# Optimization experiments

Measured on AMD Instinct MI355X. Metric: run time of the kernel, lower is better.

Reference implementation:

```python
import jax, jax.numpy as jnp
import numpy as np

D_MODEL = 1024
NUM_HEADS = 16
D_HEAD = D_MODEL // NUM_HEADS


def setup_inputs() -> dict:
    key = jax.random.key(0)
    ks = jax.random.split(key, 9)
    s = 1.0 / np.sqrt(D_MODEL)
    x = jax.random.normal(ks[0], (2, 2048, D_MODEL), dtype=jnp.float32)
    # Linear layers: weight [out, in] (torch convention), bias [out]
    w_q = jax.random.uniform(ks[1], (D_MODEL, D_MODEL), jnp.float32, -s, s)
    b_q = jax.random.uniform(ks[2], (D_MODEL,), jnp.float32, -s, s)
    w_k = jax.random.uniform(ks[3], (D_MODEL, D_MODEL), jnp.float32, -s, s)
    b_k = jax.random.uniform(ks[4], (D_MODEL,), jnp.float32, -s, s)
    w_v = jax.random.uniform(ks[5], (D_MODEL, D_MODEL), jnp.float32, -s, s)
    b_v = jax.random.uniform(ks[6], (D_MODEL,), jnp.float32, -s, s)
    w_o = jax.random.uniform(ks[7], (D_MODEL, D_MODEL), jnp.float32, -s, s)
    b_o = jax.random.uniform(ks[8], (D_MODEL,), jnp.float32, -s, s)
    return {"x": x, "w_q": w_q, "b_q": b_q, "w_k": w_k, "b_k": b_k,
            "w_v": w_v, "b_v": b_v, "w_o": w_o, "b_o": b_o}


def _split_heads(t, b, s):
    # [b, s, d_model] -> [b, h, s, d_head]
    return t.reshape(b, s, NUM_HEADS, D_HEAD).transpose(0, 2, 1, 3)


def reference(x, w_q, b_q, w_k, b_k, w_v, b_v, w_o, b_o):
    b, s, _ = x.shape
    q = _split_heads(x @ w_q.T + b_q, b, s)
    k = _split_heads(x @ w_k.T + b_k, b, s)
    v = _split_heads(x @ w_v.T + b_v, b, s)
    scores = jnp.einsum('bhid,bhjd->bhij', q, k) / jnp.sqrt(jnp.float32(D_HEAD)).astype(x.dtype)
    attn = jax.nn.softmax(scores, axis=-1)
    out = jnp.einsum('bhij,bhjd->bhid', attn, v)
    out = out.transpose(0, 2, 1, 3).reshape(b, s, D_MODEL)
    return out @ w_o.T + b_o
```

## Files before the change

### kernel.cpp

```cpp
#include <hip/hip_runtime.h>
#include <cstddef>
#include <cstdint>
#include <cmath>

#define NH   16
#define DH   64
#define SLEN 2048
#define DM   1024

typedef __bf16          bf16x8   __attribute__((ext_vector_type(8)));
typedef float           f32x4    __attribute__((ext_vector_type(4)));
typedef unsigned short  ushort8  __attribute__((ext_vector_type(8)));
typedef unsigned short  ushort4v __attribute__((ext_vector_type(4)));

__device__ __forceinline__ unsigned short f2bf(float x) {
    union { float f; unsigned u; } v; v.f = x;
    unsigned r = v.u + 0x7fffu + ((v.u >> 16) & 1u);
    return (unsigned short)(r >> 16);
}
__device__ __forceinline__ float bf2f(unsigned short h) {
    union { unsigned u; float f; } v; v.u = ((unsigned)h) << 16;
    return v.f;
}

__device__ __forceinline__ f32x4 mfma16(ushort8 a, ushort8 b, f32x4 c) {
    return __builtin_amdgcn_mfma_f32_16x16x32_bf16(
        __builtin_bit_cast(bf16x8, a), __builtin_bit_cast(bf16x8, b), c, 0, 0, 0);
}

__global__ __launch_bounds__(256)
void convert_hilo(const float* __restrict__ x,
                  const float* __restrict__ wq, const float* __restrict__ wk,
                  const float* __restrict__ wv, const float* __restrict__ wo,
                  unsigned short* __restrict__ xh, unsigned short* __restrict__ xl,
                  unsigned short* __restrict__ wh, unsigned short* __restrict__ wl)
{
    const unsigned c = blockIdx.x * 256 + threadIdx.x;
    const float* src;
    unsigned short *dh, *dl;
    size_t off;
    if (c < 1048576u) {
        src = x; dh = xh; dl = xl; off = c;
    } else {
        unsigned t = c - 1048576u;
        unsigned wsel = t >> 18;
        off = t & 262143u;
        src  = (wsel == 0) ? wq : (wsel == 1) ? wk : (wsel == 2) ? wv : wo;
        dh = wh + ((size_t)wsel << 20);
        dl = wl + ((size_t)wsel << 20);
    }
    float4 v = *(const float4*)(src + off * 4);
    float a[4] = {v.x, v.y, v.z, v.w};
    ushort4v h, l;
    #pragma unroll
    for (int i = 0; i < 4; ++i) {
        unsigned short hi = f2bf(a[i]);
        h[i] = hi;
        l[i] = f2bf(a[i] - bf2f(hi));
    }
    *(ushort4v*)(dh + off * 4) = h;
    *(ushort4v*)(dl + off * 4) = l;
}

template<int MODE>
__global__ __launch_bounds__(256, 1)
void gemm_split(const unsigned short* __restrict__ Ahi, const unsigned short* __restrict__ Alo,
                const unsigned short* __restrict__ Whi, const unsigned short* __restrict__ Wlo,
                const float* __restrict__ bias, const float scale, float* __restrict__ outF,
                unsigned short* __restrict__ outH, unsigned short* __restrict__ outL)
{
    constexpr int K = DM;
    __shared__ __align__(16) char smem[40960];
    auto sAh = (unsigned short(*)[40])(smem);
    auto sAl = (unsigned short(*)[40])(smem + 10240);
    auto sBh = (unsigned short(*)[40])(smem + 20480);
    auto sBl = (unsigned short(*)[40])(smem + 30720);

    const int tid  = threadIdx.x;
    const int bm   = blockIdx.x * 128;
    const int bn   = blockIdx.y * 128;
    const int wid  = tid >> 6;
    const int lane = tid & 63;
    const int wm   = (wid >> 1) * 64;
    const int wn   = (wid & 1) * 64;

    const int r0 = tid >> 2;
    const int c0 = (tid & 3) * 8;

    const unsigned short* pAh0 = Ahi + (size_t)(bm + r0) * K + c0;
    const unsigned short* pAl0 = Alo + (size_t)(bm + r0) * K + c0;
    const unsigned short* pBh0 = Whi + (size_t)(bn + r0) * K + c0;
    const unsigned short* pBl0 = Wlo + (size_t)(bn + r0) * K + c0;
    const size_t rstep = (size_t)64 * K;

    ushort8 vah0 = *(const ushort8*)(pAh0), vah1 = *(const ushort8*)(pAh0 + rstep);
    ushort8 val0 = *(const ushort8*)(pAl0), val1 = *(const ushort8*)(pAl0 + rstep);
    ushort8 vbh0 = *(const ushort8*)(pBh0), vbh1 = *(const ushort8*)(pBh0 + rstep);
    ushort8 vbl0 = *(const ushort8*)(pBl0), vbl1 = *(const ushort8*)(pBl0 + rstep);

    f32x4 acc[4][4];
    #pragma unroll
    for (int i = 0; i < 4; ++i)
        #pragma unroll
        for (int j = 0; j < 4; ++j)
            acc[i][j] = (f32x4)0.0f;

    const int fr = lane & 15;
    const int kq = (lane >> 4) * 8;

    for (int k0 = 0; k0 < K; k0 += 32) {
        __syncthreads();
        *(ushort8*)&sAh[r0][c0]      = vah0;  *(ushort8*)&sAh[r0 + 64][c0] = vah1;
        *(ushort8*)&sAl[r0][c0]      = val0;  *(ushort8*)&sAl[r0 + 64][c0] = val1;
        *(ushort8*)&sBh[r0][c0]      = vbh0;  *(ushort8*)&sBh[r0 + 64][c0] = vbh1;
        *(ushort8*)&sBl[r0][c0]      = vbl0;  *(ushort8*)&sBl[r0 + 64][c0] = vbl1;
        __syncthreads();

        if (k0 + 32 < K) {
            const int kn = k0 + 32;
            vah0 = *(const ushort8*)(pAh0 + kn);  vah1 = *(const ushort8*)(pAh0 + rstep + kn);
            val0 = *(const ushort8*)(pAl0 + kn);  val1 = *(const ushort8*)(pAl0 + rstep + kn);
            vbh0 = *(const ushort8*)(pBh0 + kn);  vbh1 = *(const ushort8*)(pBh0 + rstep + kn);
            vbl0 = *(const ushort8*)(pBl0 + kn);  vbl1 = *(const ushort8*)(pBl0 + rstep + kn);
        }

        ushort8 afh[4], afl[4], bfh[4], bfl[4];
        #pragma unroll
        for (int i = 0; i < 4; ++i) {
            afh[i] = *(const ushort8*)&sAh[wm + i * 16 + fr][kq];
            afl[i] = *(const ushort8*)&sAl[wm + i * 16 + fr][kq];
            bfh[i] = *(const ushort8*)&sBh[wn + i * 16 + fr][kq];
            bfl[i] = *(const ushort8*)&sBl[wn + i * 16 + fr][kq];
        }

        #pragma unroll
        for (int i = 0; i < 4; ++i)
            #pragma unroll
            for (int j = 0; j < 4; ++j) {
                acc[i][j] = mfma16(afh[i], bfh[j], acc[i][j]);
                acc[i][j] = mfma16(afh[i], bfl[j], acc[i][j]);
                acc[i][j] = mfma16(afl[i], bfh[j], acc[i][j]);
            }
    }

    if (MODE == 2) {
        float (*sT)[132] = (float(*)[132])smem;
        const int bb2 = bm >> 11;
        const int sm  = bm & 2047;
        #pragma unroll
        for (int ph = 0; ph < 2; ++ph) {
            __syncthreads();
            if ((wid & 1) == ph) {
                #pragma unroll
                for (int j = 0; j < 4; ++j) {
                    const float bs = bias[bn + ph * 64 + j * 16 + fr];
                    #pragma unroll
                    for (int i = 0; i < 4; ++i) {
                        float4 v4;
                        v4.x = acc[i][j][0] + bs;
                        v4.y = acc[i][j][1] + bs;
                        v4.z = acc[i][j][2] + bs;
                        v4.w = acc[i][j][3] + bs;
                        *(float4*)&sT[j * 16 + fr][wm + i * 16 + (lane >> 4) * 4] = v4;
                    }
                }
            }
            __syncthreads();
            #pragma unroll
            for (int half = 0; half < 2; ++half) {
                const int r  = (tid >> 3) + half * 32;
                const int cc = (tid & 7) * 16;
                const int n  = bn + ph * 64 + r;
                const size_t gb = ((((size_t)bb2 * NH + (n >> 6)) * DH) + (n & 63)) * SLEN + sm + cc;
                #pragma unroll
                for (int u = 0; u < 2; ++u) {
                    float4 f0 = *(const float4*)&sT[r][cc + u * 8];
                    float4 f1 = *(const float4*)&sT[r][cc + u * 8 + 4];
                    float fe[8] = {f0.x, f0.y, f0.z, f0.w, f1.x, f1.y, f1.z, f1.w};
                    ushort8 hv, lv;
                    #pragma unroll
                    for (int e = 0; e < 8; ++e) {
                        const unsigned short vh = f2bf(fe[e]);
                        hv[e] = vh;
                        lv[e] = f2bf(fe[e] - bf2f(vh));
                    }
                    *(ushort8*)(outH + gb + u * 8) = hv;
                    *(ushort8*)(outL + gb + u * 8) = lv;
                }
            }
        }
        return;
    }

    #pragma unroll
    for (int j = 0; j < 4; ++j) {
        const int n = bn + wn + j * 16 + fr;
        const float bs = bias[n];
        #pragma unroll
        for (int i = 0; i < 4; ++i) {
            #pragma unroll
            for (int q = 0; q < 4; ++q) {
                const int m = bm + wm + i * 16 + (lane >> 4) * 4 + q;
                const float v = (acc[i][j][q] + bs) * scale;
                if (MODE == 0) {
                    outF[(size_t)m * DM + n] = v;
                } else {
                    const int bb = m >> 11, s = m & 2047, hh = n >> 6, dd = n & 63;
                    const size_t idx = ((((size_t)bb * NH + hh) * SLEN) + s) * DH + dd;
                    const unsigned short vh = f2bf(v);
                    outH[idx] = vh;
                    outL[idx] = f2bf(v - bf2f(vh));
                }
            }
        }
    }
}

__global__ __launch_bounds__(256, 5)
void flash_attn_mfma(const unsigned short* __restrict__ Qh, const unsigned short* __restrict__ Ql,
                     const unsigned short* __restrict__ Kh, const unsigned short* __restrict__ Kl,
                     const unsigned short* __restrict__ Vth, const unsigned short* __restrict__ Vtl,
                     unsigned short* __restrict__ Ohi, unsigned short* __restrict__ Olo)
{
    __shared__ unsigned short sKh[32][72], sKl[32][72];
    __shared__ unsigned short sVh[64][40], sVl[64][40];
    __shared__ float sP[4][16][36];

    const int tid  = threadIdx.x;
    const int wid  = tid >> 6;
    const int lane = tid & 63;
    const int fr   = lane & 15;
    const int g    = lane >> 4;
    const int kq   = g * 8;
    const int q0   = blockIdx.x * 64;
    const int h    = blockIdx.y;
    const int b    = blockIdx.z;
    const size_t hb = (((size_t)b) * NH + h) * (size_t)SLEN * DH;

    const int kr = tid & 31, kc = (tid >> 5) * 8;
    const int vr = tid >> 2, vc = (tid & 3) * 8;

    ushort8 qh[2], ql[2];
    {
        const size_t qbase = hb + (size_t)(q0 + wid * 16 + fr) * DH;
        qh[0] = *(const ushort8*)&Qh[qbase + kq];
        qh[1] = *(const ushort8*)&Qh[qbase + 32 + kq];
        ql[0] = *(const ushort8*)&Ql[qbase + kq];
        ql[1] = *(const ushort8*)&Ql[qbase + 32 + kq];
    }

    float mx[4], li[4];
    f32x4 acc[4];
    #pragma unroll
    for (int r = 0; r < 4; ++r) { mx[r] = -INFINITY; li[r] = 0.0f; }
    #pragma unroll
    for (int j = 0; j < 4; ++j) acc[j] = (f32x4)0.0f;

    for (int t = 0; t < SLEN / 32; ++t) {
        __syncthreads();
        {
            const size_t kb = hb + (size_t)(t * 32 + kr) * DH + kc;
            *(ushort8*)&sKh[kr][kc] = *(const ushort8*)&Kh[kb];
            *(ushort8*)&sKl[kr][kc] = *(const ushort8*)&Kl[kb];
            const size_t vb = hb + (size_t)vr * SLEN + t * 32 + vc;
            *(ushort8*)&sVh[vr][vc] = *(const ushort8*)&Vth[vb];
            *(ushort8*)&sVl[vr][vc] = *(const ushort8*)&Vtl[vb];
        }
        __syncthreads();

        f32x4 s[2];
        s[0] = (f32x4)0.0f; s[1] = (f32x4)0.0f;
        #pragma unroll
        for (int j = 0; j < 2; ++j) {
            #pragma unroll
            for (int ks = 0; ks < 2; ++ks) {
                ushort8 kfh = *(const ushort8*)&sKh[j * 16 + fr][ks * 32 + kq];
                ushort8 kfl = *(const ushort8*)&sKl[j * 16 + fr][ks * 32 + kq];
                s[j] = mfma16(qh[ks], kfh, s[j]);
                s[j] = mfma16(qh[ks], kfl, s[j]);
                s[j] = mfma16(ql[ks], kfh, s[j]);
            }
        }

        float p[4][2];
        #pragma unroll
        for (int r = 0; r < 4; ++r) {
            const float v0 = s[0][r], v1 = s[1][r];
            float rm = fmaxf(v0, v1);
            #pragma unroll
            for (int off = 1; off < 16; off <<= 1)
                rm = fmaxf(rm, __shfl_xor(rm, off));
            const float mn   = fmaxf(mx[r], rm);
            const float corr = __expf(mx[r] - mn);
            mx[r] = mn;
            p[r][0] = __expf(v0 - mn);
            p[r][1] = __expf(v1 - mn);
            float rs = p[r][0] + p[r][1];
            #pragma unroll
            for (int off = 1; off < 16; off <<= 1)
                rs += __shfl_xor(rs, off);
            li[r] = li[r] * corr + rs;
            #pragma unroll
            for (int jd = 0; jd < 4; ++jd) acc[jd][r] *= corr;
        }

        #pragma unroll
        for (int r = 0; r < 4; ++r)
            #pragma unroll
            for (int j = 0; j < 2; ++j)
                sP[wid][g * 4 + r][j * 16 + fr] = p[r][j];

        {
            float4 pa = *(const float4*)&sP[wid][fr][kq];
            float4 pb = *(const float4*)&sP[wid][fr][kq + 4];
            float pe[8] = {pa.x, pa.y, pa.z, pa.w, pb.x, pb.y, pb.z, pb.w};
            ushort8 ph, pl;
            #pragma unroll
            for (int e = 0; e < 8; ++e) {
                const unsigned short hh2 = f2bf(pe[e]);
                ph[e] = hh2;
                pl[e] = f2bf(pe[e] - bf2f(hh2));
            }
            #pragma unroll
            for (int jd = 0; jd < 4; ++jd) {
                ushort8 vfh = *(const ushort8*)&sVh[jd * 16 + fr][kq];
                ushort8 vfl = *(const ushort8*)&sVl[jd * 16 + fr][kq];
                acc[jd] = mfma16(ph, vfh, acc[jd]);
                acc[jd] = mfma16(ph, vfl, acc[jd]);
                acc[jd] = mfma16(pl, vfh, acc[jd]);
            }
        }
    }

    #pragma unroll
    for (int r = 0; r < 4; ++r) {
        const float inv = 1.0f / li[r];
        const int q = q0 + wid * 16 + g * 4 + r;
        const size_t base = ((size_t)b * SLEN + q) * DM + h * DH;
        #pragma unroll
        for (int jd = 0; jd < 4; ++jd) {
            const float v = acc[jd][r] * inv;
            const unsigned short hh2 = f2bf(v);
            Ohi[base + jd * 16 + fr] = hh2;
            Olo[base + jd * 16 + fr] = f2bf(v - bf2f(hh2));
        }
    }
}

extern "C" void kernel_launch(void* const* d_in, const int* in_sizes, int n_in,
                              void* d_out, int out_size, void* d_ws, size_t ws_size,
                              hipStream_t stream)
{
    const float* x   = (const float*)d_in[0];
    const float* w_q = (const float*)d_in[1];
    const float* b_q = (const float*)d_in[2];
    const float* w_k = (const float*)d_in[3];
    const float* b_k = (const float*)d_in[4];
    const float* w_v = (const float*)d_in[5];
    const float* b_v = (const float*)d_in[6];
    const float* w_o = (const float*)d_in[7];
    const float* b_o = (const float*)d_in[8];
    float* out = (float*)d_out;

    char* w = (char*)d_ws;
    const size_t MB = 1024 * 1024;
    unsigned short* xh  = (unsigned short*)(w);
    unsigned short* xl  = (unsigned short*)(w + 8  * MB);
    unsigned short* wh  = (unsigned short*)(w + 16 * MB);
    unsigned short* wl  = (unsigned short*)(w + 24 * MB);
    unsigned short* Qh  = (unsigned short*)(w + 32 * MB);
    unsigned short* Ql  = (unsigned short*)(w + 40 * MB);
    unsigned short* Kh  = (unsigned short*)(w + 48 * MB);
    unsigned short* Kl  = (unsigned short*)(w + 56 * MB);
    unsigned short* Vth = (unsigned short*)(w + 64 * MB);
    unsigned short* Vtl = (unsigned short*)(w + 72 * MB);

    convert_hilo<<<8192, 256, 0, stream>>>(x, w_q, w_k, w_v, w_o, xh, xl, wh, wl);

    dim3 gg(2 * SLEN / 128, DM / 128);
    gemm_split<1><<<gg, 256, 0, stream>>>(xh, xl, wh + 0 * 1048576, wl + 0 * 1048576, b_q, 0.125f, nullptr, Qh, Ql);
    gemm_split<1><<<gg, 256, 0, stream>>>(xh, xl, wh + 1 * 1048576, wl + 1 * 1048576, b_k, 1.0f,   nullptr, Kh, Kl);
    gemm_split<2><<<gg, 256, 0, stream>>>(xh, xl, wh + 2 * 1048576, wl + 2 * 1048576, b_v, 1.0f,   nullptr, Vth, Vtl);

    dim3 ga(SLEN / 64, NH, 2);
    flash_attn_mfma<<<ga, 256, 0, stream>>>(Qh, Ql, Kh, Kl, Vth, Vtl, xh, xl);

    gemm_split<0><<<gg, 256, 0, stream>>>(xh, xl, wh + 3 * 1048576, wl + 3 * 1048576, b_o, 1.0f, out, nullptr, nullptr);
}
```

Before: 464.9 us.

## Stage Q/K projection epilogue through LDS, pad K tile, use packed bf16 convert

The head-split projection epilogue (MODE 1) now writes biased, scaled results into a shared-memory tile and then emits coalesced 16-byte hi/lo bf16 stores per row, replacing scattered 2-byte stores. The attention kernel pads the K shared tile rows from 72 to 88 elements, presumably to change LDS bank mapping. The P hi/lo split uses the hardware v_cvt_pk_bf16_f32 instruction on pairs instead of software rounding. This adds extra syncthreads and LDS traffic in the epilogue, and assumes the packed convert rounds the same way as the software version.

```diff
diff --git a/kernel.cpp b/kernel.cpp
--- a/kernel.cpp
+++ b/kernel.cpp
@@ -12,6 +12,7 @@
 typedef float           f32x4    __attribute__((ext_vector_type(4)));
 typedef unsigned short  ushort8  __attribute__((ext_vector_type(8)));
 typedef unsigned short  ushort4v __attribute__((ext_vector_type(4)));
+typedef unsigned int    uint4v   __attribute__((ext_vector_type(4)));
 
 __device__ __forceinline__ unsigned short f2bf(float x) {
     union { float f; unsigned u; } v; v.f = x;
@@ -22,8 +23,17 @@
     union { unsigned u; float f; } v; v.u = ((unsigned)h) << 16;
     return v.f;
 }
+__device__ __forceinline__ unsigned cvt_pk_bf16(float a, float b) {
+    unsigned r;
+    asm("v_cvt_pk_bf16_f32 %0, %1, %2" : "=v"(r) : "v"(a), "v"(b));
+    return r;
+}
 
 __device__ __forceinline__ f32x4 mfma16(ushort8 a, ushort8 b, f32x4 c) {
+    return __builtin_amdgcn_mfma_f32_16x16x32_bf16(
+        __builtin_bit_cast(bf16x8, a), __builtin_bit_cast(bf16x8, b), c, 0, 0, 0);
+}
+__device__ __forceinline__ f32x4 mfma16u(uint4v a, ushort8 b, f32x4 c) {
     return __builtin_amdgcn_mfma_f32_16x16x32_bf16(
         __builtin_bit_cast(bf16x8, a), __builtin_bit_cast(bf16x8, b), c, 0, 0, 0);
 }
@@ -143,10 +153,52 @@
             }
     }
 
+    const int bb2 = bm >> 11;
+    const int sm  = bm & 2047;
+
+    if (MODE == 1) {
+        float (*sT)[68] = (float(*)[68])smem;
+        #pragma unroll
+        for (int ph = 0; ph < 2; ++ph) {
+            __syncthreads();
+            if ((wid & 1) == ph) {
+                #pragma unroll
+                for (int j = 0; j < 4; ++j) {
+                    const float bs = bias[bn + ph * 64 + j * 16 + fr];
+                    #pragma unroll
+                    for (int i = 0; i < 4; ++i)
+                        #pragma unroll
+                        for (int q = 0; q < 4; ++q)
+                            sT[wm + i * 16 + (lane >> 4) * 4 + q][j * 16 + fr] =
+                                (acc[i][j][q] + bs) * scale;
+                }
+            }
+            __syncthreads();
+            const int head = (bn + ph * 64) >> 6;
+            const int r  = tid >> 1;
+            const int cc = (tid & 1) * 32;
+            const size_t gb = ((((size_t)bb2 * NH + head) * SLEN) + sm + r) * DH + cc;
+            #pragma unroll
+            for (int u = 0; u < 4; ++u) {
+                float4 f0 = *(const float4*)&sT[r][cc + u * 8];
+                float4 f1 = *(const float4*)&sT[r][cc + u * 8 + 4];
+                float fe[8] = {f0.x, f0.y, f0.z, f0.w, f1.x, f1.y, f1.z, f1.w};
+                ushort8 hv, lv;
+                #pragma unroll
+                for (int e = 0; e < 8; ++e) {
+                    const unsigned short vh = f2bf(fe[e]);
+                    hv[e] = vh;
+                    lv[e] = f2bf(fe[e] - bf2f(vh));
+                }
+                *(ushort8*)(outH + gb + u * 8) = hv;
+                *(ushort8*)(outL + gb + u * 8) = lv;
+            }
+        }
+        return;
+    }
+
     if (MODE == 2) {
         float (*sT)[132] = (float(*)[132])smem;
-        const int bb2 = bm >> 11;
-        const int sm  = bm & 2047;
         #pragma unroll
         for (int ph = 0; ph < 2; ++ph) {
             __syncthreads();
@@ -201,16 +253,7 @@
             #pragma unroll
             for (int q = 0; q < 4; ++q) {
                 const int m = bm + wm + i * 16 + (lane >> 4) * 4 + q;
-                const float v = (acc[i][j][q] + bs) * scale;
-                if (MODE == 0) {
-                    outF[(size_t)m * DM + n] = v;
-                } else {
-                    const int bb = m >> 11, s = m & 2047, hh = n >> 6, dd = n & 63;
-                    const size_t idx = ((((size_t)bb * NH + hh) * SLEN) + s) * DH + dd;
-                    const unsigned short vh = f2bf(v);
-                    outH[idx] = vh;
-                    outL[idx] = f2bf(v - bf2f(vh));
-                }
+                outF[(size_t)m * DM + n] = (acc[i][j][q] + bs) * scale;
             }
         }
     }
@@ -222,7 +265,7 @@
                      const unsigned short* __restrict__ Vth, const unsigned short* __restrict__ Vtl,
                      unsigned short* __restrict__ Ohi, unsigned short* __restrict__ Olo)
 {
-    __shared__ unsigned short sKh[32][72], sKl[32][72];
+    __shared__ unsigned short sKh[32][88], sKl[32][88];
     __shared__ unsigned short sVh[64][40], sVl[64][40];
     __shared__ float sP[4][16][36];
 
@@ -314,20 +357,22 @@
             float4 pa = *(const float4*)&sP[wid][fr][kq];
             float4 pb = *(const float4*)&sP[wid][fr][kq + 4];
             float pe[8] = {pa.x, pa.y, pa.z, pa.w, pb.x, pb.y, pb.z, pb.w};
-            ushort8 ph, pl;
-            #pragma unroll
-            for (int e = 0; e < 8; ++e) {
-                const unsigned short hh2 = f2bf(pe[e]);
-                ph[e] = hh2;
-                pl[e] = f2bf(pe[e] - bf2f(hh2));
+            uint4v ph, pl;
+            #pragma unroll
+            for (int e = 0; e < 4; ++e) {
+                const unsigned hp = cvt_pk_bf16(pe[2 * e], pe[2 * e + 1]);
+                const float r0 = __uint_as_float(hp << 16);
+                const float r1 = __uint_as_float(hp & 0xffff0000u);
+                ph[e] = hp;
+                pl[e] = cvt_pk_bf16(pe[2 * e] - r0, pe[2 * e + 1] - r1);
             }
             #pragma unroll
             for (int jd = 0; jd < 4; ++jd) {
                 ushort8 vfh = *(const ushort8*)&sVh[jd * 16 + fr][kq];
                 ushort8 vfl = *(const ushort8*)&sVl[jd * 16 + fr][kq];
-                acc[jd] = mfma16(ph, vfh, acc[jd]);
-                acc[jd] = mfma16(ph, vfl, acc[jd]);
-                acc[jd] = mfma16(pl, vfh, acc[jd]);
+                acc[jd] = mfma16u(ph, vfh, acc[jd]);
+                acc[jd] = mfma16u(ph, vfl, acc[jd]);
+                acc[jd] = mfma16u(pl, vfh, acc[jd]);
             }
         }
     }
```

New measurement: 470.6 us. No clear change (+1.2%).
